# Optimization experiments

Hardware: AMD Instinct MI355X
Metric: run time of the kernel (lower is better)

The kernel has to match this reference:

```python
import jax, jax.numpy as jnp
import numpy as np

HID = 256
NL = 4
NC = 5
SPACE = 16


def _grid_sample(feat, grid):
    # feat [B,C,H,W]; grid [B,Hg,Wg,2] in [-1,1]; bilinear, align_corners=True, zeros padding
    B, C, H, W = feat.shape
    x = (grid[..., 0] + 1.0) * 0.5 * (W - 1)
    y = (grid[..., 1] + 1.0) * 0.5 * (H - 1)
    x0f = jnp.floor(x)
    y0f = jnp.floor(y)
    wx1 = x - x0f
    wy1 = y - y0f

    def corner(yf, xf, wgt):
        valid = (xf >= 0) & (xf <= W - 1) & (yf >= 0) & (yf <= H - 1)
        xi = jnp.clip(xf, 0, W - 1).astype(jnp.int32)
        yi = jnp.clip(yf, 0, H - 1).astype(jnp.int32)
        v = jax.vmap(lambda f, yy, xx: f[:, yy, xx])(feat, yi, xi)  # [B,C,Hg,Wg]
        return v * (wgt * valid.astype(feat.dtype))[:, None]

    return (corner(y0f, x0f, (1 - wy1) * (1 - wx1))
            + corner(y0f, x0f + 1, (1 - wy1) * wx1)
            + corner(y0f + 1, x0f, wy1 * (1 - wx1))
            + corner(y0f + 1, x0f + 1, wy1 * wx1))


def _conv(x, w, b, pad):
    y = jax.lax.conv_general_dilated(x, w, (1, 1), ((pad, pad), (pad, pad)),
                                     dimension_numbers=('NCHW', 'OIHW', 'NCHW'))
    return y + b[None, :, None, None]


def _resize_ac(x, oh, ow):
    # bilinear resize with align_corners=True
    B, C, H, W = x.shape
    ys = jnp.linspace(0.0, H - 1.0, oh)
    xs = jnp.linspace(0.0, W - 1.0, ow)
    y0 = jnp.floor(ys).astype(jnp.int32)
    y1 = jnp.minimum(y0 + 1, H - 1)
    x0 = jnp.floor(xs).astype(jnp.int32)
    x1 = jnp.minimum(x0 + 1, W - 1)
    wy = (ys - y0)[None, None, :, None]
    wx = (xs - x0)[None, None, None, :]
    top = x[:, :, y0, :] * (1 - wy) + x[:, :, y1, :] * wy
    return top[:, :, :, x0] * (1 - wx) + top[:, :, :, x1] * wx


def _mlp(x, w1, b1, w2, b2):
    # 2-layer MLP, dropout is identity at inference
    return jax.nn.relu(x @ w1 + b1) @ w2 + b2


def setup_inputs() -> dict:
    key = jax.random.key(0)
    ks = jax.random.split(key, 16)
    B, H, W = 8, 512, 512

    def rn(k, shape, s=0.02):
        return jax.random.normal(k, shape, jnp.float32) * s

    return {
        'images': jax.random.normal(ks[0], (B, 3, H, W), jnp.float32),
        'feat0': jax.random.normal(ks[1], (B, HID, 128, 128), jnp.float32),
        'feat1': jax.random.normal(ks[2], (B, HID, 64, 64), jnp.float32),
        'feat2': jax.random.normal(ks[3], (B, HID, 32, 32), jnp.float32),
        'feat3': jax.random.normal(ks[4], (B, HID, 16, 16), jnp.float32),
        'mask_feat': jax.random.normal(ks[5], (B, HID, 128, 128), jnp.float32),
        'o': jax.random.normal(ks[6], (B, 16, 16, 768), jnp.float32),
        'dw1': rn(ks[7], (768, HID)), 'db1': jnp.zeros((HID,), jnp.float32),
        'dw2': rn(ks[8], (HID, 8)), 'db2': jnp.zeros((8,), jnp.float32),
        'cw1': rn(ks[9], (HID, HID)), 'cb1': jnp.zeros((HID,), jnp.float32),
        'cw2': rn(ks[10], (HID, NC + 1)), 'cb2': jnp.zeros((NC + 1,), jnp.float32),
        'conv_w': rn(ks[11], (HID, HID * NL, 3, 3)), 'conv_b': jnp.zeros((HID,), jnp.float32),
        'mw1': rn(ks[12], (HID, HID, 3, 3)), 'mb1': jnp.zeros((HID,), jnp.float32),
        'bn_g': jnp.ones((HID,), jnp.float32), 'bn_b': jnp.zeros((HID,), jnp.float32),
        'bn_m': jnp.zeros((HID,), jnp.float32), 'bn_v': jnp.ones((HID,), jnp.float32),
        'mw2': rn(ks[13], (1, HID, 1, 1)), 'mb2': jnp.zeros((1,), jnp.float32),
    }


def reference(images, feat0, feat1, feat2, feat3, mask_feat, o,
              dw1, db1, dw2, db2, cw1, cb1, cw2, cb2, conv_w, conv_b,
              mw1, mb1, bn_g, bn_b, bn_m, bn_v, mw2, mb2):
    B, _, H, W = images.shape
    ny = int(np.ceil(H / SPACE))
    nx = int(np.ceil(W / SPACE))
    # AnchorPoints: meshgrid 'xy', scaled by space, shifted by half-cell origin
    gx, gy = jnp.meshgrid(jnp.arange(nx, dtype=jnp.float32), jnp.arange(ny, dtype=jnp.float32))
    origin = jnp.array([(W % SPACE) or SPACE, (H % SPACE) or SPACE], jnp.float32) / 2
    anchors = jnp.stack([gx, gy], -1) * SPACE + origin  # [ny,nx,2] (x,y)

    # learned offsets: MLP then pixel-shuffle style 16x16x8 -> 32x32x2
    d = _mlp(o, dw1, db1, dw2, db2)  # [B,16,16,8]
    d = d.reshape(B, 16, 16, 2, 2, 2).transpose(0, 1, 3, 2, 4, 5).reshape(B, 32, 32, 2)
    prop = anchors[None] + d  # deformed proposals [B,32,32,2]

    feats = [feat0, feat1, feat2, feat3]
    strides = [4, 8, 16, 32]
    rois = []
    for f, s in zip(feats, strides):
        fh, fw = f.shape[2], f.shape[3]
        grid = 2.0 * prop / s / jnp.array([fw, fh], jnp.float32) - 1.0
        rois.append(_grid_sample(f, grid))
    roi = jnp.concatenate(rois, 1)  # [B, HID*NL, 32, 32]
    roi = _conv(roi, conv_w, conv_b, 1).transpose(0, 2, 3, 1)  # [B,32,32,HID]
    logits = _mlp(roi, cw1, cb1, cw2, cb2)  # [B,32,32,NC+1]

    # mask head: conv3x3 -> BN(eval) -> ReLU -> conv1x1(pad=1) -> bilinear upsample (align_corners=True)
    m = _conv(mask_feat, mw1, mb1, 1)
    m = m * (bn_g * jax.lax.rsqrt(bn_v + 1e-5))[None, :, None, None] \
        + (bn_b - bn_m * bn_g * jax.lax.rsqrt(bn_v + 1e-5))[None, :, None, None]
    m = jax.nn.relu(m)
    m = _conv(m, mw2, mb2, 1)  # 1x1 conv with padding=1 -> [B,1,130,130] (as in source)
    masks = _resize_ac(m, H, W)  # [B,1,H,W]

    return (prop.reshape(B, -1, 2), logits.reshape(B, -1, NC + 1), masks)
```

## Files before the change

kernel.cpp:

```cpp
#include <hip/hip_runtime.h>
#include <hip/hip_bf16.h>
#include <cstdint>
#include <cstddef>

using bf16x8 = __attribute__((ext_vector_type(8))) short;
using f32x4  = __attribute__((ext_vector_type(4))) float;

static constexpr size_t PART_OFF = 4194308;
static constexpr size_t WT_OFF   = 16777220;
static constexpr size_t WTR_SH   = (size_t)294912 * 8;
static constexpr size_t WTM_SH   = (size_t)73728 * 8;
static constexpr size_t M2P_OFF  = WT_OFF + (WTR_SH + WTM_SH) / 2;

__device__ __forceinline__ uint32_t pk2(float a, float b) {
  __hip_bfloat162 h = __float22bfloat162_rn(make_float2(a, b));
  union { __hip_bfloat162 h; uint32_t u; } c; c.h = h;
  return c.u;
}

__device__ __forceinline__ void gld16(const void* g, void* l) {
  __builtin_amdgcn_global_load_lds(
      (const __attribute__((address_space(1))) void*)g,
      (__attribute__((address_space(3))) void*)l, 16, 0, 0);
}

__device__ __forceinline__ bf16x8 ld_bf8(const uint4* p) {
  union { uint4 u; bf16x8 v; } c; c.u = *p; return c.v;
}

#define CBAR(N) do { \
    asm volatile("s_waitcnt vmcnt(" #N ")" ::: "memory"); \
    __builtin_amdgcn_sched_barrier(0); \
    __builtin_amdgcn_s_barrier(); \
    __builtin_amdgcn_sched_barrier(0); } while (0)

__global__ __launch_bounds__(256) void k_prep_w(
    const float* __restrict__ conv_w, const float* __restrict__ mw1,
    short* __restrict__ wTr, short* __restrict__ wTm, float* __restrict__ zp) {
  __shared__ float sm[16 * 292];
  int t = threadIdx.x;
  int bid = blockIdx.x;
  if (bid == 0 && t < 4) zp[t] = 0.f;
  bool is_m = (bid >= 512);
  int b2 = is_m ? (bid - 512) : bid;
  int kidx = is_m ? (b2 & 7) : (b2 & 31);
  int cog  = is_m ? (b2 >> 3) : (b2 >> 5);
  const float* src = is_m ? mw1 : conv_w;
  short* dst = is_m ? wTm : wTr;
  int CI = is_m ? 256 : 1024;
  int ci0 = kidx * 32;
  int co0 = cog * 16;
  for (int e = t; e < 4608; e += 256) {
    int row = e / 288, pos = e - row * 288;
    sm[row * 292 + pos] = src[((size_t)(co0 + row) * CI + ci0) * 9 + pos];
  }
  __syncthreads();
  int nb = cog >> 3, cofrag = cog & 7;
  for (int e = t; e < 576; e += 256) {
    int tap = e >> 6, kg = (e >> 4) & 3, lr = e & 15;
    float v[8];
#pragma unroll
    for (int j = 0; j < 8; ++j) v[j] = sm[lr * 292 + (kg * 8 + j) * 9 + tap];
    uint4 pk = make_uint4(pk2(v[0], v[1]), pk2(v[2], v[3]),
                          pk2(v[4], v[5]), pk2(v[6], v[7]));
    size_t chunk = ((size_t)(kidx * 2 + nb) * 9 + tap) * 512
                 + cofrag * 64 + kg * 16 + lr;
    *(uint4*)&dst[chunk * 8] = pk;
  }
}

__global__ __launch_bounds__(256) void k_prop(
    const float* __restrict__ o,
    const float* __restrict__ dw1, const float* __restrict__ db1,
    const float* __restrict__ dw2, const float* __restrict__ db2,
    float* __restrict__ prop) {
  __shared__ float o_lds[4 * 768];
  __shared__ float h_lds[4 * 256];
  int t = threadIdx.x;
  int bid = blockIdx.x;
  int b = bid >> 6;
  int rem = bid & 63;
  int i = rem >> 2;
  int j0 = (rem & 3) * 4;
  const float* obase = o + ((size_t)(b * 16 + i) * 16 + j0) * 768;
  for (int e = t; e < 4 * 768; e += 256) o_lds[e] = obase[e];
  __syncthreads();
  float h0 = 0.f, h1 = 0.f, h2 = 0.f, h3 = 0.f;
  for (int k = 0; k < 768; ++k) {
    float w = dw1[k * 256 + t];
    h0 = fmaf(o_lds[k], w, h0);
    h1 = fmaf(o_lds[768 + k], w, h1);
    h2 = fmaf(o_lds[1536 + k], w, h2);
    h3 = fmaf(o_lds[2304 + k], w, h3);
  }
  float bb = db1[t];
  h_lds[t]        = fmaxf(h0 + bb, 0.f);
  h_lds[256 + t]  = fmaxf(h1 + bb, 0.f);
  h_lds[512 + t]  = fmaxf(h2 + bb, 0.f);
  h_lds[768 + t]  = fmaxf(h3 + bb, 0.f);
  __syncthreads();
  if (t < 32) {
    int pos = t >> 3;
    int c   = t & 7;
    float acc = db2[c];
    const float* hp = h_lds + pos * 256;
    for (int k = 0; k < 256; ++k) acc = fmaf(hp[k], dw2[k * 8 + c], acc);
    int p = c >> 2, q = (c >> 1) & 1, cc = c & 1;
    int row = 2 * i + p;
    int col = 2 * (j0 + pos) + q;
    float anchor = (cc == 0) ? ((float)col * 16.f + 8.f) : ((float)row * 16.f + 8.f);
    prop[((size_t)(b * 32 + row) * 32 + col) * 2 + cc] = anchor + acc;
  }
}

__global__ __launch_bounds__(256) void k_sample(
    const float* __restrict__ f0, const float* __restrict__ f1,
    const float* __restrict__ f2, const float* __restrict__ f3,
    const float* __restrict__ prop, uint4* __restrict__ bfR) {
  int py = blockIdx.x;
  int l  = blockIdx.y;
  int b  = blockIdx.z;
  int t  = threadIdx.x;
  int xq = t & 31;
  int cq = t >> 5;
  const float* f = (l == 0) ? f0 : (l == 1) ? f1 : (l == 2) ? f2 : f3;
  int fsz = 128 >> l;
  float s = (float)(4 << l);

  size_t pidx = ((size_t)b * 32 + py) * 32 + xq;
  float px = prop[pidx * 2 + 0];
  float pv = prop[pidx * 2 + 1];
  float gx = 2.f * px / s / (float)fsz - 1.f;
  float gy = 2.f * pv / s / (float)fsz - 1.f;
  float x = (gx + 1.f) * 0.5f * (float)(fsz - 1);
  float y = (gy + 1.f) * 0.5f * (float)(fsz - 1);
  float x0f = floorf(x), y0f = floorf(y);
  float wx1 = x - x0f, wy1 = y - y0f;

  int off[4];
  float wgt[4];
#pragma unroll
  for (int cy = 0; cy < 2; ++cy) {
#pragma unroll
    for (int cx = 0; cx < 2; ++cx) {
      float xf = x0f + (float)cx;
      float yf = y0f + (float)cy;
      float w = (cy ? wy1 : (1.f - wy1)) * (cx ? wx1 : (1.f - wx1));
      bool valid = (xf >= 0.f) && (xf <= (float)(fsz - 1)) &&
                   (yf >= 0.f) && (yf <= (float)(fsz - 1));
      int xi = (int)fminf(fmaxf(xf, 0.f), (float)(fsz - 1));
      int yi = (int)fminf(fmaxf(yf, 0.f), (float)(fsz - 1));
      off[cy * 2 + cx] = yi * fsz + xi;
      wgt[cy * 2 + cx] = valid ? w : 0.f;
    }
  }
  const float* fb = f + (size_t)b * 256 * fsz * fsz;
#pragma unroll
  for (int i = 0; i < 4; ++i) {
    int cgl = i * 8 + cq;
    float v[8];
#pragma unroll
    for (int j = 0; j < 8; ++j) {
      const float* fc = fb + (size_t)(cgl * 8 + j) * fsz * fsz;
      v[j] = wgt[0] * fc[off[0]] + wgt[1] * fc[off[1]] +
             wgt[2] * fc[off[2]] + wgt[3] * fc[off[3]];
    }
    bfR[(((size_t)b * 128 + l * 32 + cgl) * 32 + py) * 32 + xq] =
        make_uint4(pk2(v[0], v[1]), pk2(v[2], v[3]),
                   pk2(v[4], v[5]), pk2(v[6], v[7]));
  }
}

__global__ __launch_bounds__(256) void k_cvt(const float* __restrict__ mf,
                                             uint4* __restrict__ bfA) {
  int d = blockIdx.x * 256 + threadIdx.x;
  int x = d & 127, y = (d >> 7) & 127, cg = (d >> 14) & 31, b = d >> 19;
  const float* src = mf + (((size_t)(b * 256 + cg * 8)) << 14) + (y << 7) + x;
  float v[8];
#pragma unroll
  for (int j = 0; j < 8; ++j) v[j] = src[(size_t)j << 14];
  bfA[d] = make_uint4(pk2(v[0], v[1]), pk2(v[2], v[3]),
                      pk2(v[4], v[5]), pk2(v[6], v[7]));
}

__global__ __launch_bounds__(512, 2) void k_roi_mfma(
    const uint4* __restrict__ bfR, const short* __restrict__ wTr,
    float* __restrict__ part) {
  __shared__ __align__(16) short A_s[2][1408 * 8];
  __shared__ __align__(16) short B_s[4608 * 8];
  int t = threadIdx.x;
  int lane = t & 63, wv = t >> 6, wm = wv >> 1, wn = wv & 1;
  int kg = lane >> 4, lr = lane & 15;
  int bid = blockIdx.x;
  int nb = bid & 1;
  int mi = (bid >> 1) & 31;
  int b = mi >> 2, yt = mi & 3;
  int ks = bid >> 6;

  f32x4 acc[4][4];
#pragma unroll
  for (int m = 0; m < 4; ++m)
#pragma unroll
    for (int n = 0; n < 4; ++n) acc[m][n] = {0.f, 0.f, 0.f, 0.f};

  bf16x8 Af[2][4], Bf[2][4];

  const uint4* aptr[3];
  int astep[3], aldst[3];
  bool aon[3];
#pragma unroll
  for (int i = 0; i < 3; ++i) {
    int wq = wv + 8 * i;
    aon[i] = wq < 22;
    int c = wq * 64 + lane;
    int pxi = c >> 2, slot = c & 3;
    int r = pxi / 34;
    int x = pxi - r * 34 - 1;
    int y = yt * 8 + r - 1;
    int cg4 = slot ^ ((pxi >> 1) & 3);
    bool ok = (r < 10) && (x >= 0) && (x < 32) && (y >= 0) && (y < 32);
    long chunk = ok ? (long)((((b * 128 + ks * 32 + cg4) * 32 + y) * 32) + x) : -1L;
    aptr[i] = bfR + chunk;
    astep[i] = ok ? 4096 : 0;
    aldst[i] = wq * 512;
  }
  const size_t BKC = (size_t)4608 * 8;
  const short* bbase = wTr + ((size_t)(ks * 8) * 2 + nb) * BKC;

#define ROI_ISSUE_A(BUF)                                         \
  {                                                              \
    _Pragma("unroll")                                            \
    for (int i = 0; i < 3; ++i)                                  \
      if (aon[i]) {                                              \
        gld16(aptr[i], &A_s[BUF][aldst[i]]);                     \
        aptr[i] += astep[i];                                     \
      }                                                          \
  }
#define ROI_ISSUE_H1(KC)                                         \
  {                                                              \
    const short* bk = bbase + (size_t)(KC) * 2 * BKC;            \
    _Pragma("unroll")                                            \
    for (int j = 0; j < 5; ++j) {                                \
      int w = wv + 8 * j;                                        \
      gld16(bk + (w * 64 + lane) * 8, &B_s[w * 512]);            \
    }                                                            \
  }
#define ROI_ISSUE_H2(KC)                                         \
  {                                                              \
    const short* bk = bbase + (size_t)(KC) * 2 * BKC;            \
    _Pragma("unroll")                                            \
    for (int j = 0; j < 4; ++j) {                                \
      int w = wv + 8 * j;                                        \
      gld16(bk + (2560 + w * 64 + lane) * 8,                     \
            &B_s[20480 + w * 512]);                              \
    }                                                            \
  }

#define ROI_LOADF(PB, TAP)                                                        \
  {                                                                               \
    int ky = (TAP) / 3, kx = (TAP) - ky * 3;                                      \
    _Pragma("unroll")                                                             \
    for (int n = 0; n < 4; ++n)                                                   \
      Bf[PB][n] = *(const bf16x8*)&B_s[((((TAP) * 8 + wn * 4 + n) * 4 + kg) * 16  \
                                        + lr) * 8];                               \
    _Pragma("unroll")                                                             \
    for (int m = 0; m < 4; ++m) {                                                 \
      int pb = wm * 64 + m * 16;                                                  \
      int px = ((pb >> 5) + ky) * 34 + (pb & 31) + lr + kx;                       \
      Af[PB][m] = *(const bf16x8*)&As[(px * 4 + ((kg ^ (px >> 1)) & 3)) * 8];     \
    }                                                                             \
  }
#define ROI_MMA(PB)                                                               \
  {                                                                               \
    _Pragma("unroll")                                                             \
    for (int m = 0; m < 4; ++m)                                                   \
      _Pragma("unroll")                                                           \
      for (int n = 0; n < 4; ++n)                                                 \
        acc[m][n] = __builtin_amdgcn_mfma_f32_16x16x32_bf16(Af[PB][m], Bf[PB][n], \
                                                            acc[m][n], 0, 0, 0);  \
  }
#define ROI_REGION(T0, T1)                                                        \
  {                                                                               \
    ROI_LOADF(0, T0);                                                             \
    _Pragma("unroll")                                                             \
    for (int tp = (T0); tp < (T1); ++tp) {                                        \
      if (tp + 1 < (T1)) { ROI_LOADF((tp + 1) & 1, tp + 1); }                     \
      ROI_MMA(tp & 1);                                                            \
    }                                                                             \
  }

  ROI_ISSUE_H1(0);
  ROI_ISSUE_A(0);
  __syncthreads();

  for (int kc = 0; kc < 7; ++kc) {
    int buf = kc & 1;
    const short* As = A_s[buf];
    ROI_ISSUE_H2(kc);
    ROI_ISSUE_A(buf ^ 1);
    __builtin_amdgcn_s_setprio(1);
    ROI_REGION(0, 5);
    __builtin_amdgcn_s_setprio(0);
    CBAR(2);
    ROI_ISSUE_H1(kc + 1);
    __builtin_amdgcn_s_setprio(1);
    ROI_REGION(5, 9);
    __builtin_amdgcn_s_setprio(0);
    CBAR(0);
  }
  {
    const short* As = A_s[1];
    ROI_ISSUE_H2(7);
    __builtin_amdgcn_s_setprio(1);
    ROI_REGION(0, 5);
    __builtin_amdgcn_s_setprio(0);
    CBAR(0);
    __builtin_amdgcn_s_setprio(1);
    ROI_REGION(5, 9);
    __builtin_amdgcn_s_setprio(0);
  }
#pragma unroll
  for (int m = 0; m < 4; ++m)
#pragma unroll
    for (int r = 0; r < 4; ++r) {
      int p = wm * 64 + m * 16 + kg * 4 + r;
      int y = yt * 8 + (p >> 5), x = p & 31;
      float* dst = part + (size_t)ks * 2097152 + (((size_t)b * 32 + y) * 32 + x) * 256
                        + nb * 128 + wn * 64 + lr;
#pragma unroll
      for (int n = 0; n < 4; ++n) dst[n * 16] = acc[m][n][r];
    }
}

__global__ __launch_bounds__(256) void k_mlp(
    const float* __restrict__ part, const float* __restrict__ conv_b,
    const float* __restrict__ cw1, const float* __restrict__ cb1,
    const float* __restrict__ cw2, const float* __restrict__ cb2,
    float* __restrict__ logits) {
  __shared__ float v[1024];
  __shared__ float h[1024];
  int t = threadIdx.x;
  size_t base = (size_t)blockIdx.x * 1024;
  const size_t CH = (size_t)8192 * 256;
  for (int e = t; e < 1024; e += 256) {
    float s = part[base + e] + part[CH + base + e] +
              part[2 * CH + base + e] + part[3 * CH + base + e];
    v[e] = s + conv_b[e & 255];
  }
  __syncthreads();
  float a0 = cb1[t], a1 = a0, a2 = a0, a3 = a0;
  for (int k = 0; k < 256; ++k) {
    float w = cw1[k * 256 + t];
    a0 = fmaf(v[k], w, a0);
    a1 = fmaf(v[256 + k], w, a1);
    a2 = fmaf(v[512 + k], w, a2);
    a3 = fmaf(v[768 + k], w, a3);
  }
  h[t]       = fmaxf(a0, 0.f);
  h[256 + t] = fmaxf(a1, 0.f);
  h[512 + t] = fmaxf(a2, 0.f);
  h[768 + t] = fmaxf(a3, 0.f);
  __syncthreads();
  if (t < 24) {
    int pos = t / 6, c = t - 6 * pos;
    float acc = cb2[c];
    const float* hp = h + pos * 256;
    for (int k = 0; k < 256; ++k) acc = fmaf(hp[k], cw2[k * 6 + c], acc);
    logits[((size_t)blockIdx.x * 4 + pos) * 6 + c] = acc;
  }
}

__global__ __launch_bounds__(512, 2) void k_mask_mfma(
    const uint4* __restrict__ bfA, const short* __restrict__ wTm,
    const float* __restrict__ mb1,
    const float* __restrict__ bn_g, const float* __restrict__ bn_b,
    const float* __restrict__ bn_m, const float* __restrict__ bn_v,
    const float* __restrict__ mw2, float* __restrict__ m2p) {
  __shared__ __align__(16) short B_s[4608 * 8];
  int t = threadIdx.x;
  int lane = t & 63, wv = t >> 6, wm = wv >> 1, wn = wv & 1;
  int kg = lane >> 4, lr = lane & 15;
  int bid = blockIdx.x;
  int nb = bid & 1;
  int tile = bid >> 1;
  int b = tile >> 6, yt = tile & 63;
  int wmx = wm & 1, wmr = wm >> 1;

  f32x4 acc[4][4];
#pragma unroll
  for (int m = 0; m < 4; ++m)
#pragma unroll
    for (int n = 0; n < 4; ++n) acc[m][n] = {0.f, 0.f, 0.f, 0.f};

  bf16x8 Af[2][4], Bf[2][4];
  const bf16x8 z8 = {0, 0, 0, 0, 0, 0, 0, 0};

  const uint4* akc = bfA + ((size_t)(b * 32 + kg) << 14);
  int yb = 2 * yt + wmr - 1;
  int xl = wmx * 64 + lr - 1;

  const size_t BKC = (size_t)4608 * 8;
  const short* bbase = wTm + (size_t)nb * BKC;

#define MSK_ISSUE_H1(KC)                                         \
  {                                                              \
    const short* bk = bbase + (size_t)(KC) * 2 * BKC;            \
    _Pragma("unroll")                                            \
    for (int j = 0; j < 5; ++j) {                                \
      int w = wv + 8 * j;                                        \
      gld16(bk + (w * 64 + lane) * 8, &B_s[w * 512]);            \
    }                                                            \
  }
#define MSK_ISSUE_H2(KC)                                         \
  {                                                              \
    const short* bk = bbase + (size_t)(KC) * 2 * BKC;            \
    _Pragma("unroll")                                            \
    for (int j = 0; j < 4; ++j) {                                \
      int w = wv + 8 * j;                                        \
      gld16(bk + (2560 + w * 64 + lane) * 8,                     \
            &B_s[20480 + w * 512]);                              \
    }                                                            \
  }

#define MSK_LOADF(PB, TAP)                                                        \
  {                                                                               \
    const int ky = (TAP) / 3, kx = (TAP) - ky * 3;                                \
    _Pragma("unroll")                                                             \
    for (int n = 0; n < 4; ++n)                                                   \
      Bf[PB][n] = *(const bf16x8*)&B_s[((((TAP) * 8 + wn * 4 + n) * 4 + kg) * 16  \
                                        + lr) * 8];                               \
    int y = yb + ky;                                                              \
    if ((unsigned)y < 128u) {                                                     \
      const uint4* ay = akc + y * 128;                                            \
      _Pragma("unroll")                                                           \
      for (int m = 0; m < 4; ++m) {                                               \
        int x = xl + m * 16 + kx;                                                 \
        if (m == 0 && kx == 0) x = (x < 0) ? 0 : x;                               \
        if (m == 3 && kx == 2) x = (x > 127) ? 127 : x;                           \
        Af[PB][m] = ld_bf8(ay + x);                                               \
      }                                                                           \
      if (kx == 0) { if (wmx == 0) Af[PB][0] = (lr == 0)  ? z8 : Af[PB][0]; }     \
      if (kx == 2) { if (wmx == 1) Af[PB][3] = (lr == 15) ? z8 : Af[PB][3]; }     \
    } else {                                                                      \
      _Pragma("unroll")                                                           \
      for (int m = 0; m < 4; ++m) Af[PB][m] = z8;                                 \
    }                                                                             \
  }
#define MSK_MMA(PB)                                                               \
  {                                                                               \
    _Pragma("unroll")                                                             \
    for (int m = 0; m < 4; ++m)                                                   \
      _Pragma("unroll")                                                           \
      for (int n = 0; n < 4; ++n)                                                 \
        acc[m][n] = __builtin_amdgcn_mfma_f32_16x16x32_bf16(Af[PB][m], Bf[PB][n], \
                                                            acc[m][n], 0, 0, 0);  \
  }
#define MSK_REGION(T0, T1)                                                        \
  {                                                                               \
    MSK_LOADF(0, T0);                                                             \
    _Pragma("unroll")                                                             \
    for (int tp = (T0); tp < (T1); ++tp) {                                        \
      if (tp + 1 < (T1)) { MSK_LOADF((tp + 1) & 1, tp + 1); }                     \
      MSK_MMA(tp & 1);                                                            \
    }                                                                             \
  }

  MSK_ISSUE_H1(0);
  CBAR(0);

  for (int kc = 0; kc < 8; ++kc) {
    MSK_ISSUE_H2(kc);
    __builtin_amdgcn_s_setprio(1);
    MSK_REGION(0, 5);
    __builtin_amdgcn_s_setprio(0);
    CBAR(0);
    if (kc < 7) MSK_ISSUE_H1(kc + 1);
    __builtin_amdgcn_s_setprio(1);
    MSK_REGION(5, 9);
    __builtin_amdgcn_s_setprio(0);
    CBAR(0);
    akc += 65536;
  }

  float sc[4], sh[4], w2v[4], b1[4];
#pragma unroll
  for (int n = 0; n < 4; ++n) {
    int co = nb * 128 + wn * 64 + n * 16 + lr;
    float s = bn_g[co] * rsqrtf(bn_v[co] + 1e-5f);
    sc[n] = s;
    sh[n] = bn_b[co] - bn_m[co] * s;
    b1[n] = mb1[co];
    w2v[n] = mw2[co];
  }
  float* red = (float*)&B_s[0];
#pragma unroll
  for (int m = 0; m < 4; ++m)
#pragma unroll
    for (int r = 0; r < 4; ++r) {
      int p = wmr * 128 + wmx * 64 + m * 16 + kg * 4 + r;
      float s = 0.f;
#pragma unroll
      for (int n = 0; n < 4; ++n) {
        float z = fmaf(acc[m][n][r] + b1[n], sc[n], sh[n]);
        s = fmaf(w2v[n], fmaxf(z, 0.f), s);
      }
      red[p * 32 + wn * 16 + lr] = s;
    }
  __syncthreads();
  if (t < 256) {
    float s = 0.f;
#pragma unroll
    for (int q = 0; q < 32; ++q) s += red[t * 32 + q];
    int y = 2 * yt + (t >> 7);
    int x = t & 127;
    m2p[(size_t)nb * 131072 + ((size_t)b * 128 + y) * 128 + x] = s;
  }
}

__global__ __launch_bounds__(256) void k_resize(const float* __restrict__ m2p,
                                                const float* __restrict__ mb2,
                                                float* __restrict__ masks) {
  int idx = blockIdx.x * 256 + threadIdx.x;
  int b = idx >> 18;
  int rem = idx & 262143;
  int y = rem >> 9;
  int x = rem & 511;
  const float SC = 129.0f / 511.0f;
  float sy = (float)y * SC;
  float sx = (float)x * SC;
  float y0f = floorf(sy), x0f = floorf(sx);
  int y0 = (int)y0f, x0 = (int)x0f;
  int y1 = min(y0 + 1, 129), x1 = min(x0 + 1, 129);
  float wy = sy - y0f, wx = sx - x0f;
  float base = mb2[0];
  const float* p0 = m2p + (size_t)b * 16384;
  const float* p1 = m2p + 131072 + (size_t)b * 16384;

  auto corner = [&](int yy, int xx) -> float {
    if (yy >= 1 && yy <= 128 && xx >= 1 && xx <= 128) {
      int o2 = (yy - 1) * 128 + (xx - 1);
      return base + p0[o2] + p1[o2];
    }
    return base;
  };
  float tv = corner(y0, x0) * (1.f - wx) + corner(y0, x1) * wx;
  float bv = corner(y1, x0) * (1.f - wx) + corner(y1, x1) * wx;
  masks[idx] = tv * (1.f - wy) + bv * wy;
}

extern "C" void kernel_launch(void* const* d_in, const int* in_sizes, int n_in,
                              void* d_out, int out_size, void* d_ws, size_t ws_size,
                              hipStream_t stream) {
  (void)in_sizes; (void)n_in; (void)out_size; (void)ws_size;
  const float* f0        = (const float*)d_in[1];
  const float* f1        = (const float*)d_in[2];
  const float* f2        = (const float*)d_in[3];
  const float* f3        = (const float*)d_in[4];
  const float* mask_feat = (const float*)d_in[5];
  const float* o         = (const float*)d_in[6];
  const float* dw1       = (const float*)d_in[7];
  const float* db1       = (const float*)d_in[8];
  const float* dw2       = (const float*)d_in[9];
  const float* db2       = (const float*)d_in[10];
  const float* cw1       = (const float*)d_in[11];
  const float* cb1       = (const float*)d_in[12];
  const float* cw2       = (const float*)d_in[13];
  const float* cb2       = (const float*)d_in[14];
  const float* conv_w    = (const float*)d_in[15];
  const float* conv_b    = (const float*)d_in[16];
  const float* mw1       = (const float*)d_in[17];
  const float* mb1       = (const float*)d_in[18];
  const float* bn_g      = (const float*)d_in[19];
  const float* bn_b      = (const float*)d_in[20];
  const float* bn_m      = (const float*)d_in[21];
  const float* bn_v      = (const float*)d_in[22];
  const float* mw2       = (const float*)d_in[23];
  const float* mb2       = (const float*)d_in[24];

  float* ws   = (float*)d_ws;
  uint4* bf   = (uint4*)(ws + 4);
  float* part = ws + PART_OFF;
  short* wTr  = (short*)(ws + WT_OFF);
  short* wTm  = wTr + WTR_SH;
  float* m2p  = ws + M2P_OFF;

  float* out_prop   = (float*)d_out;
  float* out_logits = out_prop + (size_t)8 * 1024 * 2;
  float* out_masks  = out_logits + (size_t)8 * 1024 * 6;

  hipLaunchKernelGGL(k_prep_w, dim3(640), dim3(256), 0, stream,
                     conv_w, mw1, wTr, wTm, ws);
  hipLaunchKernelGGL(k_prop, dim3(512), dim3(256), 0, stream,
                     o, dw1, db1, dw2, db2, out_prop);
  hipLaunchKernelGGL(k_sample, dim3(32, 4, 8), dim3(256), 0, stream,
                     f0, f1, f2, f3, out_prop, bf);
  hipLaunchKernelGGL(k_roi_mfma, dim3(256), dim3(512), 0, stream,
                     bf, wTr, part);
  hipLaunchKernelGGL(k_mlp, dim3(2048), dim3(256), 0, stream,
                     part, conv_b, cw1, cb1, cw2, cb2, out_logits);
  hipLaunchKernelGGL(k_cvt, dim3(16384), dim3(256), 0, stream,
                     mask_feat, bf);
  hipLaunchKernelGGL(k_mask_mfma, dim3(1024), dim3(512), 0, stream,
                     bf, wTm, mb1, bn_g, bn_b, bn_m, bn_v, mw2, m2p);
  hipLaunchKernelGGL(k_resize, dim3(8192), dim3(256), 0, stream,
                     m2p, mb2, out_masks);
}
```

Baseline: 351.0 us.

## Restructure mask conv MFMA: full-N tiles, LDS-staged swizzled A, double-buffered pipeline

The mask 3x3 conv kernel now computes all 256 output channels per block instead of splitting N across two blocks, so each input row tile is loaded once. Activations are staged into LDS with global_load_lds using an XOR swizzle and reused across the three kx taps, replacing per-lane direct global loads. B and A tiles are double-buffered per (kc, ky) step. The two-partial reduction in resize disappears, and the weight prep layout for the mask weights changes to match. In exchange, blocks hold more accumulators (8x4 tiles) and use more LDS, and half as many blocks are launched, which may lower occupancy.

```diff
diff --git a/kernel.cpp b/kernel.cpp
--- a/kernel.cpp
+++ b/kernel.cpp
@@ -22,10 +22,6 @@
   __builtin_amdgcn_global_load_lds(
       (const __attribute__((address_space(1))) void*)g,
       (__attribute__((address_space(3))) void*)l, 16, 0, 0);
-}
-
-__device__ __forceinline__ bf16x8 ld_bf8(const uint4* p) {
-  union { uint4 u; bf16x8 v; } c; c.u = *p; return c.v;
 }
 
 #define CBAR(N) do { \
@@ -55,7 +51,6 @@
     sm[row * 292 + pos] = src[((size_t)(co0 + row) * CI + ci0) * 9 + pos];
   }
   __syncthreads();
-  int nb = cog >> 3, cofrag = cog & 7;
   for (int e = t; e < 576; e += 256) {
     int tap = e >> 6, kg = (e >> 4) & 3, lr = e & 15;
     float v[8];
@@ -63,8 +58,13 @@
     for (int j = 0; j < 8; ++j) v[j] = sm[lr * 292 + (kg * 8 + j) * 9 + tap];
     uint4 pk = make_uint4(pk2(v[0], v[1]), pk2(v[2], v[3]),
                           pk2(v[4], v[5]), pk2(v[6], v[7]));
-    size_t chunk = ((size_t)(kidx * 2 + nb) * 9 + tap) * 512
-                 + cofrag * 64 + kg * 16 + lr;
+    size_t chunk;
+    if (is_m) {
+      chunk = (((size_t)kidx * 9 + tap) * 16 + cog) * 64 + kg * 16 + lr;
+    } else {
+      int nb = cog >> 3, cofrag = cog & 7;
+      chunk = ((size_t)(kidx * 2 + nb) * 9 + tap) * 512 + cofrag * 64 + kg * 16 + lr;
+    }
     *(uint4*)&dst[chunk * 8] = pk;
   }
 }
@@ -376,144 +376,137 @@
     const float* __restrict__ bn_g, const float* __restrict__ bn_b,
     const float* __restrict__ bn_m, const float* __restrict__ bn_v,
     const float* __restrict__ mw2, float* __restrict__ m2p) {
-  __shared__ __align__(16) short B_s[4608 * 8];
+  __shared__ __align__(16) short A_s[2][1040 * 8];
+  __shared__ __align__(16) short B_s[2][3072 * 8];
   int t = threadIdx.x;
-  int lane = t & 63, wv = t >> 6, wm = wv >> 1, wn = wv & 1;
+  int lane = t & 63, wv = t >> 6;
+  int wm = wv >> 2, wn = wv & 3;
   int kg = lane >> 4, lr = lane & 15;
   int bid = blockIdx.x;
-  int nb = bid & 1;
-  int tile = bid >> 1;
-  int b = tile >> 6, yt = tile & 63;
-  int wmx = wm & 1, wmr = wm >> 1;
-
-  f32x4 acc[4][4];
-#pragma unroll
-  for (int m = 0; m < 4; ++m)
+  int b = bid >> 6, yt = bid & 63;
+
+  f32x4 acc[8][4];
+#pragma unroll
+  for (int m = 0; m < 8; ++m)
 #pragma unroll
     for (int n = 0; n < 4; ++n) acc[m][n] = {0.f, 0.f, 0.f, 0.f};
 
-  bf16x8 Af[2][4], Bf[2][4];
-  const bf16x8 z8 = {0, 0, 0, 0, 0, 0, 0, 0};
-
-  const uint4* akc = bfA + ((size_t)(b * 32 + kg) << 14);
-  int yb = 2 * yt + wmr - 1;
-  int xl = wmx * 64 + lr - 1;
-
-  const size_t BKC = (size_t)4608 * 8;
-  const short* bbase = wTm + (size_t)nb * BKC;
-
-#define MSK_ISSUE_H1(KC)                                         \
-  {                                                              \
-    const short* bk = bbase + (size_t)(KC) * 2 * BKC;            \
-    _Pragma("unroll")                                            \
-    for (int j = 0; j < 5; ++j) {                                \
-      int w = wv + 8 * j;                                        \
-      gld16(bk + (w * 64 + lane) * 8, &B_s[w * 512]);            \
-    }                                                            \
-  }
-#define MSK_ISSUE_H2(KC)                                         \
-  {                                                              \
-    const short* bk = bbase + (size_t)(KC) * 2 * BKC;            \
-    _Pragma("unroll")                                            \
-    for (int j = 0; j < 4; ++j) {                                \
-      int w = wv + 8 * j;                                        \
-      gld16(bk + (2560 + w * 64 + lane) * 8,                     \
-            &B_s[20480 + w * 512]);                              \
-    }                                                            \
-  }
-
-#define MSK_LOADF(PB, TAP)                                                        \
+  int ybase[3], cxoff[3], aldst[3];
+  bool aok[3];
+#pragma unroll
+  for (int j = 0; j < 3; ++j) {
+    int c = j * 512 + t;
+    bool on = c < 1040;
+    int cc = on ? c : 0;
+    int pxi = cc >> 2, slot = cc & 3;
+    int r = pxi / 130;
+    int sx = pxi - r * 130;
+    int x = sx - 1;
+    int cg4 = slot ^ ((pxi >> 1) & 3);
+    aok[j] = on && (x >= 0) && (x < 128);
+    ybase[j] = 2 * yt + r - 1;
+    cxoff[j] = cg4 * 16384 + x;
+    aldst[j] = cc * 8;
+  }
+  int akc = (b * 32) << 14;
+
+#define MSK_ISSUE_A(BUF, KYV, AKC)                                 \
+  {                                                                \
+    _Pragma("unroll")                                              \
+    for (int j = 0; j < 3; ++j) {                                  \
+      int y = ybase[j] + (KYV);                                    \
+      bool ok = aok[j] && ((unsigned)y < 128u);                    \
+      int off = ok ? ((AKC) + cxoff[j] + y * 128) : -1;            \
+      if (j < 2 || t < 16) gld16(bfA + off, &A_s[BUF][aldst[j]]);  \
+    }                                                              \
+  }
+#define MSK_ISSUE_B(BUF, BSRC)                                     \
+  {                                                                \
+    _Pragma("unroll")                                              \
+    for (int j = 0; j < 6; ++j) {                                  \
+      int idx = j * 512 + t;                                       \
+      gld16((BSRC) + idx * 8, &B_s[BUF][idx * 8]);                 \
+    }                                                              \
+  }
+
+#define MSK_COMPUTE(BUF)                                                          \
   {                                                                               \
-    const int ky = (TAP) / 3, kx = (TAP) - ky * 3;                                \
+    const short* As = A_s[BUF];                                                   \
+    const short* Bs = B_s[BUF];                                                   \
     _Pragma("unroll")                                                             \
-    for (int n = 0; n < 4; ++n)                                                   \
-      Bf[PB][n] = *(const bf16x8*)&B_s[((((TAP) * 8 + wn * 4 + n) * 4 + kg) * 16  \
-                                        + lr) * 8];                               \
-    int y = yb + ky;                                                              \
-    if ((unsigned)y < 128u) {                                                     \
-      const uint4* ay = akc + y * 128;                                            \
-      _Pragma("unroll")                                                           \
-      for (int m = 0; m < 4; ++m) {                                               \
-        int x = xl + m * 16 + kx;                                                 \
-        if (m == 0 && kx == 0) x = (x < 0) ? 0 : x;                               \
-        if (m == 3 && kx == 2) x = (x > 127) ? 127 : x;                           \
-        Af[PB][m] = ld_bf8(ay + x);                                               \
-      }                                                                           \
-      if (kx == 0) { if (wmx == 0) Af[PB][0] = (lr == 0)  ? z8 : Af[PB][0]; }     \
-      if (kx == 2) { if (wmx == 1) Af[PB][3] = (lr == 15) ? z8 : Af[PB][3]; }     \
-    } else {                                                                      \
-      _Pragma("unroll")                                                           \
-      for (int m = 0; m < 4; ++m) Af[PB][m] = z8;                                 \
-    }                                                                             \
-  }
-#define MSK_MMA(PB)                                                               \
-  {                                                                               \
-    _Pragma("unroll")                                                             \
-    for (int m = 0; m < 4; ++m)                                                   \
+    for (int kx = 0; kx < 3; ++kx) {                                              \
+      bf16x8 Bf[4];                                                               \
       _Pragma("unroll")                                                           \
       for (int n = 0; n < 4; ++n)                                                 \
-        acc[m][n] = __builtin_amdgcn_mfma_f32_16x16x32_bf16(Af[PB][m], Bf[PB][n], \
-                                                            acc[m][n], 0, 0, 0);  \
-  }
-#define MSK_REGION(T0, T1)                                                        \
-  {                                                                               \
-    MSK_LOADF(0, T0);                                                             \
-    _Pragma("unroll")                                                             \
-    for (int tp = (T0); tp < (T1); ++tp) {                                        \
-      if (tp + 1 < (T1)) { MSK_LOADF((tp + 1) & 1, tp + 1); }                     \
-      MSK_MMA(tp & 1);                                                            \
+        Bf[n] = *(const bf16x8*)&Bs[(((kx * 16 + wn * 4 + n) * 4 + kg) * 16       \
+                                     + lr) * 8];                                  \
+      _Pragma("unroll")                                                           \
+      for (int m = 0; m < 8; ++m) {                                               \
+        int px = wm * 130 + m * 16 + lr + kx;                                     \
+        bf16x8 af = *(const bf16x8*)&As[(px * 4 + ((kg ^ (px >> 1)) & 3)) * 8];   \
+        _Pragma("unroll")                                                         \
+        for (int n = 0; n < 4; ++n)                                               \
+          acc[m][n] = __builtin_amdgcn_mfma_f32_16x16x32_bf16(af, Bf[n],          \
+                                                              acc[m][n], 0, 0, 0);\
+      }                                                                           \
     }                                                                             \
   }
 
-  MSK_ISSUE_H1(0);
+  MSK_ISSUE_A(0, 0, akc);
+  MSK_ISSUE_B(0, wTm);
   CBAR(0);
 
-  for (int kc = 0; kc < 8; ++kc) {
-    MSK_ISSUE_H2(kc);
+  int kyv = 0;
+  const short* bnext = wTm + 24576;
+  for (int s = 0; s < 24; ++s) {
+    int buf = s & 1;
+    if (s < 23) {
+      int nky = (kyv == 2) ? 0 : kyv + 1;
+      int nakc = (kyv == 2) ? akc + 65536 : akc;
+      MSK_ISSUE_A(buf ^ 1, nky, nakc);
+      MSK_ISSUE_B(buf ^ 1, bnext);
+      kyv = nky;
+      akc = nakc;
+      bnext += 24576;
+    }
     __builtin_amdgcn_s_setprio(1);
-    MSK_REGION(0, 5);
+    MSK_COMPUTE(buf);
     __builtin_amdgcn_s_setprio(0);
     CBAR(0);
-    if (kc < 7) MSK_ISSUE_H1(kc + 1);
-    __builtin_amdgcn_s_setprio(1);
-    MSK_REGION(5, 9);
-    __builtin_amdgcn_s_setprio(0);
-    CBAR(0);
-    akc += 65536;
   }
 
   float sc[4], sh[4], w2v[4], b1[4];
 #pragma unroll
   for (int n = 0; n < 4; ++n) {
-    int co = nb * 128 + wn * 64 + n * 16 + lr;
+    int co = wn * 64 + n * 16 + lr;
     float s = bn_g[co] * rsqrtf(bn_v[co] + 1e-5f);
     sc[n] = s;
     sh[n] = bn_b[co] - bn_m[co] * s;
     b1[n] = mb1[co];
     w2v[n] = mw2[co];
   }
-  float* red = (float*)&B_s[0];
-#pragma unroll
-  for (int m = 0; m < 4; ++m)
+  float* red = (float*)&B_s[0][0];
+#pragma unroll
+  for (int m = 0; m < 8; ++m)
 #pragma unroll
     for (int r = 0; r < 4; ++r) {
-      int p = wmr * 128 + wmx * 64 + m * 16 + kg * 4 + r;
+      int px = m * 16 + kg * 4 + r;
       float s = 0.f;
 #pragma unroll
       for (int n = 0; n < 4; ++n) {
         float z = fmaf(acc[m][n][r] + b1[n], sc[n], sh[n]);
         s = fmaf(w2v[n], fmaxf(z, 0.f), s);
       }
-      red[p * 32 + wn * 16 + lr] = s;
+      red[(wm * 128 + px) * 66 + wn * 16 + lr] = s;
     }
   __syncthreads();
   if (t < 256) {
     float s = 0.f;
 #pragma unroll
-    for (int q = 0; q < 32; ++q) s += red[t * 32 + q];
-    int y = 2 * yt + (t >> 7);
-    int x = t & 127;
-    m2p[(size_t)nb * 131072 + ((size_t)b * 128 + y) * 128 + x] = s;
+    for (int q = 0; q < 64; ++q) s += red[t * 66 + q];
+    int row = 2 * yt + (t >> 7);
+    int col = t & 127;
+    m2p[((size_t)b * 128 + row) * 128 + col] = s;
   }
 }
 
@@ -534,13 +527,10 @@
   float wy = sy - y0f, wx = sx - x0f;
   float base = mb2[0];
   const float* p0 = m2p + (size_t)b * 16384;
-  const float* p1 = m2p + 131072 + (size_t)b * 16384;
 
   auto corner = [&](int yy, int xx) -> float {
-    if (yy >= 1 && yy <= 128 && xx >= 1 && xx <= 128) {
-      int o2 = (yy - 1) * 128 + (xx - 1);
-      return base + p0[o2] + p1[o2];
-    }
+    if (yy >= 1 && yy <= 128 && xx >= 1 && xx <= 128)
+      return base + p0[(yy - 1) * 128 + (xx - 1)];
     return base;
   };
   float tv = corner(y0, x0) * (1.f - wx) + corner(y0, x1) * wx;
@@ -600,7 +590,7 @@
                      part, conv_b, cw1, cb1, cw2, cb2, out_logits);
   hipLaunchKernelGGL(k_cvt, dim3(16384), dim3(256), 0, stream,
                      mask_feat, bf);
-  hipLaunchKernelGGL(k_mask_mfma, dim3(1024), dim3(512), 0, stream,
+  hipLaunchKernelGGL(k_mask_mfma, dim3(512), dim3(512), 0, stream,
                      bf, wTm, mb1, bn_g, bn_b, bn_m, bn_v, mw2, m2p);
   hipLaunchKernelGGL(k_resize, dim3(8192), dim3(256), 0, stream,
                      m2p, mb2, out_masks);
```

New measurement: 333.4 us. 5.0% less time.
